# Kernel tuning notes

Measured on AMD Instinct MI355X. Metric: run time of the kernel, lower is better.

The kernel has to match this reference:

```python
import jax, jax.numpy as jnp
import numpy as np
import math

B, L, D, H, FF = 8, 4096, 1024, 16, 4
BELOW, ABOVE = 1, 1
DH = D // H


def _timing_signal(length, channels, min_ts=1.0, max_ts=10000.0):
    position = np.arange(length)
    num_timescales = channels // 2
    log_inc = math.log(max_ts / min_ts) / (num_timescales - 1)
    inv = min_ts * np.exp(np.arange(num_timescales).astype(float) * -log_inc)
    scaled = position[:, None] * inv[None, :]
    sig = np.zeros((length, channels))
    sig[:, 0::2] = np.sin(scaled)
    sig[:, 1::2] = np.cos(scaled)
    return jnp.asarray(sig[None], dtype=jnp.float32)  # [1, L, D]


def setup_inputs() -> dict:
    key = jax.random.key(0)
    ks = jax.random.split(key, 8)
    s = lambda k, sh: jax.random.normal(k, sh, jnp.float32) * 0.02
    return dict(
        X=jax.random.normal(ks[0], (B, L, D), jnp.float32),
        src_mask=jnp.zeros((B, L), jnp.bool_),  # True = padding
        pe=_timing_signal(L, D),
        Wq=s(ks[1], (D, D)), Wk=s(ks[2], (D, D)), Wv=s(ks[3], (D, D)),
        bq=jnp.zeros((D,), jnp.float32), bk=jnp.zeros((D,), jnp.float32), bv=jnp.zeros((D,), jnp.float32),
        Wo=s(ks[4], (D, D)), bo=jnp.zeros((D,), jnp.float32),
        g1=jnp.ones((D,), jnp.float32), beta1=jnp.zeros((D,), jnp.float32),
        W1=s(ks[5], (D, FF * D)), b1=jnp.zeros((FF * D,), jnp.float32),
        W2=s(ks[6], (FF * D, D)), b2=jnp.zeros((D,), jnp.float32),
        g2=jnp.ones((D,), jnp.float32), beta2=jnp.zeros((D,), jnp.float32),
    )


def _layernorm(x, g, b, eps=1e-5):
    m = x.mean(-1, keepdims=True)
    v = ((x - m) ** 2).mean(-1, keepdims=True)
    return (x - m) * jax.lax.rsqrt(v + eps) * g + b


def reference(X, src_mask, pe, Wq, Wk, Wv, bq, bk, bv, Wo, bo,
              g1, beta1, W1, b1, W2, b2, g2, beta2):
    # positional encoding (dropout is identity in eval)
    X = X + pe  # [B, L, D]

    # QKV projections -> [B, L, H, DH]
    q = (X @ Wq + bq).reshape(B, L, H, DH)
    k = (X @ Wk + bk).reshape(B, L, H, DH)
    v = (X @ Wv + bv).reshape(B, L, H, DH)

    # Banded (diagonal-window) attention: query i attends keys i-BELOW..i+ABOVE.
    Wwin = BELOW + ABOVE + 1
    idx = jnp.arange(L)[:, None] + jnp.arange(-BELOW, ABOVE + 1)[None, :]  # [L, Wwin]
    valid = (idx >= 0) & (idx < L)
    idxc = jnp.clip(idx, 0, L - 1)
    kw = k[:, idxc]  # [B, L, Wwin, H, DH]
    vw = v[:, idxc]

    scores = jnp.einsum('blhd,blwhd->bhlw', q, kw) / jnp.sqrt(jnp.float32(DH))
    key_ok = ~src_mask  # [B, L]
    allow = valid[None, :, :] & key_ok[:, idxc]  # [B, L, Wwin]
    scores = jnp.where(allow[:, None, :, :], scores, jnp.float32(-1e30))
    attn = jax.nn.softmax(scores, axis=-1)  # [B, H, L, Wwin]
    ctx = jnp.einsum('bhlw,blwhd->blhd', attn, vw).reshape(B, L, D)
    Xt = ctx @ Wo + bo

    # post-norm residual blocks (dropout identity in eval)
    X = _layernorm(X + Xt, g1, beta1)
    ffn = jnp.maximum(X @ W1 + b1, 0.0) @ W2 + b2
    X = _layernorm(X + ffn, g2, beta2)
    return X
```

## Files before the change

### kernel.cpp

```cpp
#include <hip/hip_runtime.h>
#include <hip/hip_bf16.h>

#define B_  8
#define L_  4096
#define D_  1024
#define H_  16
#define MTOT (B_*L_)
#define NFF  (4*D_)

typedef __bf16 bf16_t;
typedef float  f32x4 __attribute__((ext_vector_type(4)));
typedef __bf16 b16x8 __attribute__((ext_vector_type(8)));
typedef __bf16 b16x4 __attribute__((ext_vector_type(4)));

#define OFF_WQKVT ((size_t)0)
#define OFF_WOT   ((size_t)6291456)
#define OFF_W1T   ((size_t)8388608)
#define OFF_W2T   ((size_t)16777216)
#define OFF_BQKV  ((size_t)25165824)
#define OFF_XB    ((size_t)33554432)
#define OFF_B     ((size_t)100663296)

__global__ __launch_bounds__(256) void k_add_pe(const float* __restrict__ X,
                                                const float* __restrict__ pe,
                                                bf16_t* __restrict__ Xb)
{
    size_t i  = ((size_t)blockIdx.x * 256 + threadIdx.x) * 4;
    size_t ld = i & ((size_t)L_ * D_ - 1);
    float4 x = *(const float4*)(X + i);
    float4 p = *(const float4*)(pe + ld);
    b16x4 b;
    b[0] = (bf16_t)(x.x + p.x); b[1] = (bf16_t)(x.y + p.y);
    b[2] = (bf16_t)(x.z + p.z); b[3] = (bf16_t)(x.w + p.w);
    *(b16x4*)(Xb + i) = b;
}

__global__ __launch_bounds__(256) void k_prep(const float* __restrict__ Wq,
                                              const float* __restrict__ Wk,
                                              const float* __restrict__ Wv,
                                              const float* __restrict__ Wo,
                                              const float* __restrict__ W1,
                                              const float* __restrict__ W2,
                                              const float* __restrict__ bq,
                                              const float* __restrict__ bk,
                                              const float* __restrict__ bv,
                                              bf16_t* __restrict__ WqkvT,
                                              bf16_t* __restrict__ WoT,
                                              bf16_t* __restrict__ W1T,
                                              bf16_t* __restrict__ W2T,
                                              float* __restrict__ bqkv)
{
    const int id = blockIdx.x;
    if (id >= 12288) {
        const int i = (id - 12288) * 256 + threadIdx.x;
        if (i < 1024)       bqkv[i] = bq[i];
        else if (i < 2048)  bqkv[i] = bk[i - 1024];
        else if (i < 3072)  bqkv[i] = bv[i - 2048];
        return;
    }
    const float* src; bf16_t* dst; int K, N, t;
    if (id < 4096) {
        const int w = id >> 10; t = id & 1023; K = 1024; N = 1024;
        src = (w == 0) ? Wq : (w == 1) ? Wk : (w == 2) ? Wv : Wo;
        dst = (w < 3) ? (WqkvT + (size_t)w * 1024 * 1024) : WoT;
    } else if (id < 8192) {
        t = id - 4096; K = 1024; N = 4096; src = W1; dst = W1T;
    } else {
        t = id - 8192; K = 4096; N = 1024; src = W2; dst = W2T;
    }
    const int ntiles = N >> 5;
    const int n0 = (t % ntiles) << 5;
    const int k0 = (t / ntiles) << 5;

    __shared__ float tt[32][33];
    const int tx = threadIdx.x & 31;
    const int ty = threadIdx.x >> 5;
    #pragma unroll
    for (int i = ty; i < 32; i += 8)
        tt[i][tx] = src[(size_t)(k0 + i) * N + n0 + tx];
    __syncthreads();
    #pragma unroll
    for (int i = ty; i < 32; i += 8)
        dst[(size_t)(n0 + i) * K + k0 + tx] = (bf16_t)tt[tx][i];
}


__device__ __forceinline__ void gload_lds16(const void* g, char* lds_byte) {
    __builtin_amdgcn_global_load_lds((const __attribute__((address_space(1))) void*)g,
                                     (__attribute__((address_space(3))) void*)lds_byte,
                                     16, 0, 0);
}

#define GBAR() __builtin_amdgcn_s_barrier()
#define VM4()  asm volatile("s_waitcnt vmcnt(4)" ::: "memory")
#define VM2()  asm volatile("s_waitcnt vmcnt(2)" ::: "memory")
#define PRI(x) __builtin_amdgcn_s_setprio(x)
#define SB0()  __builtin_amdgcn_sched_barrier(0)

template<int EPI, int KC>
__global__ __launch_bounds__(512, 2) void k_g256(const bf16_t* __restrict__ A,
                                                 const bf16_t* __restrict__ Bt,
                                                 const float* __restrict__ bias,
                                                 void* __restrict__ Cv,
                                                 const int N)
{
    extern __shared__ char smem[];
    const int tid  = threadIdx.x;
    const int wave = tid >> 6;
    const int lane = tid & 63;
    const int wm   = wave >> 2;
    const int wn   = wave & 3;

    const int Nt = gridDim.x, Mt = gridDim.y;
    const int lid = blockIdx.y * Nt + blockIdx.x;
    const int xcd = lid & 7;
    const int sgl = lid >> 3;
    const int bm  = xcd * (Mt >> 3) + sgl / Nt;
    const int bn  = sgl % Nt;
    const int m0 = bm * 256, n0 = bn * 256;

    const int srow   = tid >> 3;
    const int schunk = (tid & 7) ^ (srow & 7);
    const bf16_t* agA = A  + (size_t)(m0 + srow) * KC + schunk * 8;
    const bf16_t* bgB = Bt + (size_t)(n0 + srow) * KC + schunk * 8;
    const size_t rstep = (size_t)64 * KC;
    char* ldsw = smem + wave * 1024;

    const int q  = lane >> 4, x7 = lane & 7;
    const int sl0 = (q ^ x7) << 3;
    const int sl1 = ((4 + q) ^ x7) << 3;
    const bf16_t* A0p = (const bf16_t*)(smem)         + (wm * 128 + (lane & 15)) * 64;
    const bf16_t* B0p = (const bf16_t*)(smem + 32768) + (wn * 64  + (lane & 15)) * 64;
    const bf16_t* A1p = (const bf16_t*)(smem + 65536) + (wm * 128 + (lane & 15)) * 64;
    const bf16_t* B1p = (const bf16_t*)(smem + 98304) + (wn * 64  + (lane & 15)) * 64;

    f32x4 acc[8][4] = {};
    b16x8 aF[8], bF[8];

#define STG2(gb, koff, ldsoff, pair) \
    gload_lds16(gb + (size_t)(2*(pair)+0)*rstep + (koff), ldsw + (ldsoff) + (2*(pair)+0)*8192); \
    gload_lds16(gb + (size_t)(2*(pair)+1)*rstep + (koff), ldsw + (ldsoff) + (2*(pair)+1)*8192)
#define RDA_K(P, mh, kh) { _Pragma("unroll") for (int ml = 0; ml < 4; ++ml) \
    aF[2*ml+(kh)] = *(const b16x8*)((P) + (mh)*4096 + ml*1024 + ((kh) ? sl1 : sl0)); }
#define RDB_K(P, nh, kh) { _Pragma("unroll") for (int nl = 0; nl < 2; ++nl) \
    bF[2*((nh)*2+nl)+(kh)] = *(const b16x8*)((P) + ((nh)*2+nl)*1024 + ((kh) ? sl1 : sl0)); }
#define MMK(kh, mh, nh) { _Pragma("unroll") for (int ml = 0; ml < 4; ++ml) \
    _Pragma("unroll") for (int nl = 0; nl < 2; ++nl) { \
        f32x4& c = acc[(mh)*4+ml][(nh)*2+nl]; \
        c = __builtin_amdgcn_mfma_f32_16x16x32_bf16(aF[2*ml+(kh)], bF[2*((nh)*2+nl)+(kh)], c, 0, 0, 0); } }

    #pragma unroll
    for (int i = 0; i < 4; ++i) gload_lds16(agA + (size_t)i * rstep,      ldsw + 0     + i * 8192);
    #pragma unroll
    for (int i = 0; i < 4; ++i) gload_lds16(bgB + (size_t)i * rstep,      ldsw + 32768 + i * 8192);
    #pragma unroll
    for (int i = 0; i < 4; ++i) gload_lds16(bgB + (size_t)i * rstep + 64, ldsw + 98304 + i * 8192);
    VM4();
    GBAR();
    RDA_K(A0p, 0, 0); RDB_K(B0p, 0, 0);
    RDA_K(A0p, 0, 1); RDB_K(B0p, 0, 1);
    SB0();

    int kb = 0;
    const int niter = KC >> 7;
    for (int it = 0; it < niter; ++it) {
        const int k1 = (kb +  64) & (KC - 1);
        const int k2 = (kb + 128) & (KC - 1);
        const int k3 = (kb + 192) & (KC - 1);
        STG2(agA, k1, 65536, 0);
        RDB_K(B0p, 1, 0); RDB_K(B0p, 1, 1); SB0();
        PRI(1); MMK(0,0,0); MMK(1,0,0); PRI(0); SB0();
        GBAR();
        STG2(agA, k1, 65536, 1);
        PRI(1); MMK(0,0,1); PRI(0);
        RDA_K(A0p, 1, 0); SB0();
        PRI(1); MMK(1,0,1); PRI(0);
        RDA_K(A0p, 1, 1); SB0();
        GBAR();
        STG2(bgB, k2, 32768, 0);
        PRI(1); MMK(0,1,1); MMK(1,1,1); PRI(0);
        VM2(); GBAR();
        STG2(bgB, k2, 32768, 1);
        PRI(1); MMK(0,1,0); PRI(0);
        RDA_K(A1p, 0, 0); RDB_K(B1p, 0, 0); SB0();
        PRI(1); MMK(1,1,0); PRI(0);
        RDA_K(A1p, 0, 1); RDB_K(B1p, 0, 1); SB0();
        GBAR();
        STG2(agA, k2, 0, 0);
        RDB_K(B1p, 1, 0); RDB_K(B1p, 1, 1); SB0();
        PRI(1); MMK(0,0,0); MMK(1,0,0); PRI(0); SB0();
        GBAR();
        STG2(agA, k2, 0, 1);
        PRI(1); MMK(0,0,1); PRI(0);
        RDA_K(A1p, 1, 0); SB0();
        PRI(1); MMK(1,0,1); PRI(0);
        RDA_K(A1p, 1, 1); SB0();
        GBAR();
        STG2(bgB, k3, 98304, 0);
        PRI(1); MMK(0,1,1); MMK(1,1,1); PRI(0);
        VM2(); GBAR();
        STG2(bgB, k3, 98304, 1);
        PRI(1); MMK(0,1,0); PRI(0);
        RDA_K(A0p, 0, 0); RDB_K(B0p, 0, 0); SB0();
        PRI(1); MMK(1,1,0); PRI(0);
        RDA_K(A0p, 0, 1); RDB_K(B0p, 0, 1); SB0();
        GBAR();
        kb = (kb + 128) & (KC - 1);
    }
    asm volatile("s_waitcnt vmcnt(0)" ::: "memory");

    const int rbase = m0 + wm * 128 + ((lane >> 4) << 2);
    const int cbase = n0 + wn * 64 + (lane & 15);
    #pragma unroll
    for (int mi = 0; mi < 8; ++mi) {
        #pragma unroll
        for (int ni = 0; ni < 4; ++ni) {
            const int col = cbase + ni * 16;
            const float bb = bias[col];
            #pragma unroll
            for (int r = 0; r < 4; ++r) {
                const int rowg = rbase + mi * 16 + r;
                float v = acc[mi][ni][r] + bb;
                if (EPI == 2) v = fmaxf(v, 0.0f);
                if (EPI == 0) ((float*)Cv)[(size_t)rowg * N + col] = v;
                else          ((bf16_t*)Cv)[(size_t)rowg * N + col] = (bf16_t)v;
            }
        }
    }
#undef STG2
#undef RDA_K
#undef RDB_K
#undef MMK
}

__global__ __launch_bounds__(256) void k_attn(const bf16_t* __restrict__ QKV,
                                              const unsigned char* __restrict__ mask,
                                              bf16_t* __restrict__ ctx)
{
    const int wid  = (blockIdx.x << 2) + (threadIdx.x >> 6);
    const int lane = threadIdx.x & 63;
    const int h    = wid & (H_ - 1);
    const int l    = wid >> 4;
    const int lb   = l & (L_ - 1);

    const float qv = (float)QKV[(size_t)l * 3072 + h * 64 + lane];
    float sc[3], vv[3];
    bool  ok[3];
    #pragma unroll
    for (int w = 0; w < 3; ++w) {
        const int d   = w - 1;
        const bool valid = (unsigned)(lb + d) < (unsigned)L_;
        const int dc  = valid ? d : 0;
        const size_t rb = (size_t)(l + dc) * 3072 + h * 64 + lane;
        const float kk = (float)QKV[rb + 1024];
        vv[w] = (float)QKV[rb + 2048];
        ok[w] = valid && (mask[l + dc] == 0);
        sc[w] = qv * kk;
    }
    #pragma unroll
    for (int off = 32; off; off >>= 1) {
        sc[0] += __shfl_xor(sc[0], off);
        sc[1] += __shfl_xor(sc[1], off);
        sc[2] += __shfl_xor(sc[2], off);
    }
    const float s0 = ok[0] ? sc[0] * 0.125f : -1e30f;
    const float s1 = ok[1] ? sc[1] * 0.125f : -1e30f;
    const float s2 = ok[2] ? sc[2] * 0.125f : -1e30f;
    const float mx = fmaxf(s0, fmaxf(s1, s2));
    const float e0 = __expf(s0 - mx), e1 = __expf(s1 - mx), e2 = __expf(s2 - mx);
    const float inv = 1.0f / (e0 + e1 + e2);
    const float o = (e0 * vv[0] + e1 * vv[1] + e2 * vv[2]) * inv;
    ctx[(size_t)l * 1024 + h * 64 + lane] = (bf16_t)o;
}

template<int FINAL>
__global__ __launch_bounds__(256) void k_res_ln(const bf16_t* __restrict__ Xres,
                                                const float* __restrict__ Y,
                                                const float* __restrict__ g,
                                                const float* __restrict__ beta,
                                                bf16_t* __restrict__ outB,
                                                float* __restrict__ outF)
{
    const int row = blockIdx.x;
    const int tid = threadIdx.x;
    const size_t base = (size_t)row * D_ + tid * 4;
    b16x4  xr = *(const b16x4*)(Xres + base);
    float4 y  = *(const float4*)(Y + base);
    const float t0 = (float)xr[0] + y.x, t1 = (float)xr[1] + y.y;
    const float t2 = (float)xr[2] + y.z, t3 = (float)xr[3] + y.w;
    float s = t0 + t1 + t2 + t3;
    float qq = t0*t0 + t1*t1 + t2*t2 + t3*t3;
    #pragma unroll
    for (int off = 32; off; off >>= 1) {
        s  += __shfl_xor(s, off);
        qq += __shfl_xor(qq, off);
    }
    __shared__ float red[8];
    const int wv = tid >> 6, ln = tid & 63;
    if (ln == 0) { red[wv] = s; red[wv + 4] = qq; }
    __syncthreads();
    s  = red[0] + red[1] + red[2] + red[3];
    qq = red[4] + red[5] + red[6] + red[7];
    const float mean = s * (1.0f / D_);
    const float var  = qq * (1.0f / D_) - mean * mean;
    const float rs   = rsqrtf(var + 1e-5f);
    const int c = tid * 4;
    float4 gv = *(const float4*)(g + c);
    float4 bv = *(const float4*)(beta + c);
    float o0 = (t0 - mean) * rs * gv.x + bv.x;
    float o1 = (t1 - mean) * rs * gv.y + bv.y;
    float o2 = (t2 - mean) * rs * gv.z + bv.z;
    float o3 = (t3 - mean) * rs * gv.w + bv.w;
    if (FINAL) {
        float4 o; o.x = o0; o.y = o1; o.z = o2; o.w = o3;
        *(float4*)(outF + base) = o;
    } else {
        b16x4 b; b[0] = (bf16_t)o0; b[1] = (bf16_t)o1; b[2] = (bf16_t)o2; b[3] = (bf16_t)o3;
        *(b16x4*)(outB + base) = b;
    }
}

extern "C" void kernel_launch(void* const* d_in, const int* in_sizes, int n_in,
                              void* d_out, int out_size, void* d_ws, size_t ws_size,
                              hipStream_t stream)
{
    const float* X    = (const float*)d_in[0];
    const unsigned char* mask = (const unsigned char*)d_in[1];
    const float* pe   = (const float*)d_in[2];
    const float* Wq   = (const float*)d_in[3];
    const float* Wk   = (const float*)d_in[4];
    const float* Wv   = (const float*)d_in[5];
    const float* bq   = (const float*)d_in[6];
    const float* bk   = (const float*)d_in[7];
    const float* bv   = (const float*)d_in[8];
    const float* Wo   = (const float*)d_in[9];
    const float* bo   = (const float*)d_in[10];
    const float* g1   = (const float*)d_in[11];
    const float* be1  = (const float*)d_in[12];
    const float* W1   = (const float*)d_in[13];
    const float* b1   = (const float*)d_in[14];
    const float* W2   = (const float*)d_in[15];
    const float* b2   = (const float*)d_in[16];
    const float* g2   = (const float*)d_in[17];
    const float* be2  = (const float*)d_in[18];

    static int s_attr = [](){
        (void)hipFuncSetAttribute(reinterpret_cast<const void*>(&k_g256<0,1024>),
                                  hipFuncAttributeMaxDynamicSharedMemorySize, 131072);
        (void)hipFuncSetAttribute(reinterpret_cast<const void*>(&k_g256<1,1024>),
                                  hipFuncAttributeMaxDynamicSharedMemorySize, 131072);
        (void)hipFuncSetAttribute(reinterpret_cast<const void*>(&k_g256<2,1024>),
                                  hipFuncAttributeMaxDynamicSharedMemorySize, 131072);
        (void)hipFuncSetAttribute(reinterpret_cast<const void*>(&k_g256<0,4096>),
                                  hipFuncAttributeMaxDynamicSharedMemorySize, 131072);
        return 0;
    }();
    (void)s_attr;

    char* ws = (char*)d_ws;
    bf16_t* WqkvT = (bf16_t*)(ws + OFF_WQKVT);
    bf16_t* WoT   = (bf16_t*)(ws + OFF_WOT);
    bf16_t* W1T   = (bf16_t*)(ws + OFF_W1T);
    bf16_t* W2T   = (bf16_t*)(ws + OFF_W2T);
    float*  bqkv  = (float*) (ws + OFF_BQKV);
    bf16_t* Xb    = (bf16_t*)(ws + OFF_XB);
    float*  Y     = (float*)d_out;

    const bool big = ws_size >= (size_t)234881024;

    k_add_pe<<<MTOT * D_ / 1024, 256, 0, stream>>>(X, pe, Xb);

    k_prep<<<12300, 256, 0, stream>>>(Wq, Wk, Wv, Wo, W1, W2, bq, bk, bv,
                                      WqkvT, WoT, W1T, W2T, bqkv);

    if (big) {
        bf16_t* ctx  = (bf16_t*)(ws + OFF_B);
        bf16_t* qkvc = (bf16_t*)(ws + OFF_B + 67108864);
        for (int c = 0; c < 4; ++c) {
            const size_t r0 = (size_t)c * 8192;
            k_g256<1,1024><<<dim3(3072/256, 8192/256), 512, 131072, stream>>>(
                Xb + r0*D_, WqkvT, bqkv, qkvc, 3072);
            k_attn<<<8192*H_/4, 256, 0, stream>>>(qkvc, mask + r0, ctx + r0*D_);
        }
        k_g256<0,1024><<<dim3(1024/256, MTOT/256), 512, 131072, stream>>>(ctx, WoT, bo, Y, 1024);
        k_res_ln<0><<<MTOT, 256, 0, stream>>>(Xb, Y, g1, be1, Xb, nullptr);
        bf16_t* hb = (bf16_t*)(ws + OFF_B);
        for (int c = 0; c < 2; ++c) {
            const size_t r0 = (size_t)c * 16384;
            k_g256<2,1024><<<dim3(NFF/256, 16384/256), 512, 131072, stream>>>(
                Xb + r0*D_, W1T, b1, hb, NFF);
            k_g256<0,4096><<<dim3(1024/256, 16384/256), 512, 131072, stream>>>(
                hb, W2T, b2, Y + r0*D_, 1024);
        }
        k_res_ln<1><<<MTOT, 256, 0, stream>>>(Xb, Y, g2, be2, nullptr, (float*)d_out);
    } else {
        bf16_t* qkvc = (bf16_t*)(ws + OFF_B);
        bf16_t* ctxc = (bf16_t*)(ws + OFF_B + 25165824);
        for (int b = 0; b < B_; ++b) {
            const size_t r0 = (size_t)b * L_;
            k_g256<1,1024><<<dim3(3072/256, L_/256), 512, 131072, stream>>>(
                Xb + r0*D_, WqkvT, bqkv, qkvc, 3072);
            k_attn<<<L_*H_/4, 256, 0, stream>>>(qkvc, mask + r0, ctxc);
            k_g256<0,1024><<<dim3(1024/256, L_/256), 512, 131072, stream>>>(
                ctxc, WoT, bo, Y + r0*D_, 1024);
        }
        k_res_ln<0><<<MTOT, 256, 0, stream>>>(Xb, Y, g1, be1, Xb, nullptr);
        bf16_t* hb = (bf16_t*)(ws + OFF_B);
        for (int c = 0; c < 8; ++c) {
            const size_t r0 = (size_t)c * L_;
            k_g256<2,1024><<<dim3(NFF/256, L_/256), 512, 131072, stream>>>(
                Xb + r0*D_, W1T, b1, hb, NFF);
            k_g256<0,4096><<<dim3(1024/256, L_/256), 512, 131072, stream>>>(
                hb, W2T, b2, Y + r0*D_, 1024);
        }
        k_res_ln<1><<<MTOT, 256, 0, stream>>>(Xb, Y, g2, be2, nullptr, (float*)d_out);
    }
}
```

Before: 1.338 ms.

## Restructure GEMM main loop into eight-phase ping-pong schedule with explicit LDS waits

Replaces the interleaved LDS-read/MFMA software pipeline in the 256x256 GEMM with a phased schedule. Each phase reads full-K fragments, issues global-to-LDS loads, waits on lgkmcnt, then runs a block of MFMAs between barriers. The goal is cleaner separation of memory and compute phases so waves can alternate in ping-pong fashion. The cost is many more barriers per iteration and no fragment prefetch across phases, which may expose LDS latency.

```diff
diff --git a/kernel.cpp b/kernel.cpp
--- a/kernel.cpp
+++ b/kernel.cpp
@@ -91,11 +91,12 @@
                                      16, 0, 0);
 }
 
-#define GBAR() __builtin_amdgcn_s_barrier()
-#define VM4()  asm volatile("s_waitcnt vmcnt(4)" ::: "memory")
-#define VM2()  asm volatile("s_waitcnt vmcnt(2)" ::: "memory")
-#define PRI(x) __builtin_amdgcn_s_setprio(x)
-#define SB0()  __builtin_amdgcn_sched_barrier(0)
+#define GBAR()  __builtin_amdgcn_s_barrier()
+#define VM4()   asm volatile("s_waitcnt vmcnt(4)" ::: "memory")
+#define LGKM0() asm volatile("s_waitcnt lgkmcnt(0)" ::: "memory")
+#define LGKM8() asm volatile("s_waitcnt lgkmcnt(8)" ::: "memory")
+#define PRI(x)  __builtin_amdgcn_s_setprio(x)
+#define SB0()   __builtin_amdgcn_sched_barrier(0)
 
 template<int EPI, int KC>
 __global__ __launch_bounds__(512, 2) void k_g256(const bf16_t* __restrict__ A,
@@ -140,14 +141,17 @@
 #define STG2(gb, koff, ldsoff, pair) \
     gload_lds16(gb + (size_t)(2*(pair)+0)*rstep + (koff), ldsw + (ldsoff) + (2*(pair)+0)*8192); \
     gload_lds16(gb + (size_t)(2*(pair)+1)*rstep + (koff), ldsw + (ldsoff) + (2*(pair)+1)*8192)
-#define RDA_K(P, mh, kh) { _Pragma("unroll") for (int ml = 0; ml < 4; ++ml) \
-    aF[2*ml+(kh)] = *(const b16x8*)((P) + (mh)*4096 + ml*1024 + ((kh) ? sl1 : sl0)); }
-#define RDB_K(P, nh, kh) { _Pragma("unroll") for (int nl = 0; nl < 2; ++nl) \
-    bF[2*((nh)*2+nl)+(kh)] = *(const b16x8*)((P) + ((nh)*2+nl)*1024 + ((kh) ? sl1 : sl0)); }
-#define MMK(kh, mh, nh) { _Pragma("unroll") for (int ml = 0; ml < 4; ++ml) \
+#define RDA(P, mh) { _Pragma("unroll") for (int ml = 0; ml < 4; ++ml) { \
+    aF[2*ml+0] = *(const b16x8*)((P) + (mh)*4096 + ml*1024 + sl0); \
+    aF[2*ml+1] = *(const b16x8*)((P) + (mh)*4096 + ml*1024 + sl1); } }
+#define RDB(P, nh) { _Pragma("unroll") for (int nl = 0; nl < 2; ++nl) { \
+    bF[2*((nh)*2+nl)+0] = *(const b16x8*)((P) + ((nh)*2+nl)*1024 + sl0); \
+    bF[2*((nh)*2+nl)+1] = *(const b16x8*)((P) + ((nh)*2+nl)*1024 + sl1); } }
+#define MM(mh, nh) { _Pragma("unroll") for (int ml = 0; ml < 4; ++ml) \
     _Pragma("unroll") for (int nl = 0; nl < 2; ++nl) { \
         f32x4& c = acc[(mh)*4+ml][(nh)*2+nl]; \
-        c = __builtin_amdgcn_mfma_f32_16x16x32_bf16(aF[2*ml+(kh)], bF[2*((nh)*2+nl)+(kh)], c, 0, 0, 0); } }
+        c = __builtin_amdgcn_mfma_f32_16x16x32_bf16(aF[2*ml+0], bF[2*((nh)*2+nl)+0], c, 0, 0, 0); \
+        c = __builtin_amdgcn_mfma_f32_16x16x32_bf16(aF[2*ml+1], bF[2*((nh)*2+nl)+1], c, 0, 0, 0); } }
 
     #pragma unroll
     for (int i = 0; i < 4; ++i) gload_lds16(agA + (size_t)i * rstep,      ldsw + 0     + i * 8192);
@@ -157,9 +161,6 @@
     for (int i = 0; i < 4; ++i) gload_lds16(bgB + (size_t)i * rstep + 64, ldsw + 98304 + i * 8192);
     VM4();
     GBAR();
-    RDA_K(A0p, 0, 0); RDB_K(B0p, 0, 0);
-    RDA_K(A0p, 0, 1); RDB_K(B0p, 0, 1);
-    SB0();
 
     int kb = 0;
     const int niter = KC >> 7;
@@ -167,44 +168,30 @@
         const int k1 = (kb +  64) & (KC - 1);
         const int k2 = (kb + 128) & (KC - 1);
         const int k3 = (kb + 192) & (KC - 1);
-        STG2(agA, k1, 65536, 0);
-        RDB_K(B0p, 1, 0); RDB_K(B0p, 1, 1); SB0();
-        PRI(1); MMK(0,0,0); MMK(1,0,0); PRI(0); SB0();
+        RDA(A0p, 0); RDB(B0p, 0); STG2(agA, k1, 65536, 0); LGKM8(); SB0();
+        GBAR(); LGKM0(); SB0();
+        PRI(1); MM(0, 0); PRI(0); GBAR();
+        RDB(B0p, 1);              STG2(agA, k1, 65536, 1); SB0();
+        GBAR(); LGKM0(); SB0();
+        PRI(1); MM(0, 1); PRI(0); GBAR();
+        RDA(A0p, 1);              STG2(bgB, k2, 32768, 0); SB0();
+        GBAR(); LGKM0(); SB0();
+        PRI(1); MM(1, 1); PRI(0); GBAR();
+                                  STG2(bgB, k2, 32768, 1); VM4(); SB0();
         GBAR();
-        STG2(agA, k1, 65536, 1);
-        PRI(1); MMK(0,0,1); PRI(0);
-        RDA_K(A0p, 1, 0); SB0();
-        PRI(1); MMK(1,0,1); PRI(0);
-        RDA_K(A0p, 1, 1); SB0();
+        PRI(1); MM(1, 0); PRI(0); GBAR();
+        RDA(A1p, 0); RDB(B1p, 0); STG2(agA, k2, 0, 0); LGKM8(); SB0();
+        GBAR(); LGKM0(); SB0();
+        PRI(1); MM(0, 0); PRI(0); GBAR();
+        RDB(B1p, 1);              STG2(agA, k2, 0, 1); SB0();
+        GBAR(); LGKM0(); SB0();
+        PRI(1); MM(0, 1); PRI(0); GBAR();
+        RDA(A1p, 1);              STG2(bgB, k3, 98304, 0); SB0();
+        GBAR(); LGKM0(); SB0();
+        PRI(1); MM(1, 1); PRI(0); GBAR();
+                                  STG2(bgB, k3, 98304, 1); VM4(); SB0();
         GBAR();
-        STG2(bgB, k2, 32768, 0);
-        PRI(1); MMK(0,1,1); MMK(1,1,1); PRI(0);
-        VM2(); GBAR();
-        STG2(bgB, k2, 32768, 1);
-        PRI(1); MMK(0,1,0); PRI(0);
-        RDA_K(A1p, 0, 0); RDB_K(B1p, 0, 0); SB0();
-        PRI(1); MMK(1,1,0); PRI(0);
-        RDA_K(A1p, 0, 1); RDB_K(B1p, 0, 1); SB0();
-        GBAR();
-        STG2(agA, k2, 0, 0);
-        RDB_K(B1p, 1, 0); RDB_K(B1p, 1, 1); SB0();
-        PRI(1); MMK(0,0,0); MMK(1,0,0); PRI(0); SB0();
-        GBAR();
-        STG2(agA, k2, 0, 1);
-        PRI(1); MMK(0,0,1); PRI(0);
-        RDA_K(A1p, 1, 0); SB0();
-        PRI(1); MMK(1,0,1); PRI(0);
-        RDA_K(A1p, 1, 1); SB0();
-        GBAR();
-        STG2(bgB, k3, 98304, 0);
-        PRI(1); MMK(0,1,1); MMK(1,1,1); PRI(0);
-        VM2(); GBAR();
-        STG2(bgB, k3, 98304, 1);
-        PRI(1); MMK(0,1,0); PRI(0);
-        RDA_K(A0p, 0, 0); RDB_K(B0p, 0, 0); SB0();
-        PRI(1); MMK(1,1,0); PRI(0);
-        RDA_K(A0p, 0, 1); RDB_K(B0p, 0, 1); SB0();
-        GBAR();
+        PRI(1); MM(1, 0); PRI(0); GBAR();
         kb = (kb + 128) & (KC - 1);
     }
     asm volatile("s_waitcnt vmcnt(0)" ::: "memory");
@@ -228,9 +215,9 @@
         }
     }
 #undef STG2
-#undef RDA_K
-#undef RDB_K
-#undef MMK
+#undef RDA
+#undef RDB
+#undef MM
 }
 
 __global__ __launch_bounds__(256) void k_attn(const bf16_t* __restrict__ QKV,
```

Result: no change. 1.352 ms (+1.0%).
